# Kernel tuning notes

Measured on AMD Instinct MI355X. Metric: run time of the kernel, lower is better.

The kernel has to match this reference:

```python
import jax, jax.numpy as jnp
import numpy as np

DS = 32          # decoder_size
DIM = 512        # decoder_dim
NH = 8           # num_heads
HD = DIM // NH   # head_size = 64
NE = 4           # num_enc_reshape
NC = 2           # num_classes
B = 8
L = 2            # transformer layers
FF = 4 * DIM


def _ln(x, g, b):
    m = x.mean(-1, keepdims=True)
    v = x.var(-1, keepdims=True)
    return (x - m) / jnp.sqrt(v + 1e-5) * g + b


def _pos_bias(x_emb, y_emb, pad0, pad1):
    # 2D relative position encoding gathered from embeddings, shape [S2,S2,HD]
    ix = jnp.tile(jnp.arange(DS), DS)                       # column index per pixel
    iy = jnp.repeat(jnp.arange(DS), DS)                     # row index per pixel
    xd = jnp.clip(ix[None, :] - ix[:, None], -DS, DS) + DS  # [S2,S2] in [1,2*DS-1]
    yd = jnp.clip(iy[None, :] - iy[:, None], -DS, DS) + DS
    pos = x_emb[xd] + y_emb[yd]                              # [S2,S2,HD]
    S2 = DS * DS
    p0 = jnp.broadcast_to(pad0, (NE, NE, HD))
    p1 = jnp.broadcast_to(pad1, (S2, NE, HD))
    pos_pad = jnp.concatenate([p0, p1], axis=0)              # [S,NE,HD]
    right = jnp.concatenate([jnp.transpose(p1, (1, 0, 2)), pos], axis=0)  # [S,S2,HD]
    return jnp.concatenate([pos_pad, right], axis=1)         # [S,S,HD]


def _forward(x, patches, We, be, x_emb, y_emb, pad0, pad1,
             Wq, bq, Wk, bk, Wv, bv, Wo, bo,
             ln1_g, ln1_b, ln2_g, ln2_b, W1, b1, W2, b2, Wc, bc):
    b = x.shape[0]
    # patch embedding: [B,3,H,W] -> [B,H,W,3] -> Linear(3,DIM) -> [B,S2,DIM]
    p = jnp.transpose(patches, (0, 2, 3, 1))
    px = (p @ We + be).reshape(b, -1, DIM)
    xe = x.reshape(b, NE, DIM)
    h = jnp.concatenate([xe, px], axis=1)                    # [B,S,DIM]
    pos = _pos_bias(x_emb, y_emb, pad0, pad1)                # [S,S,HD]
    scale = 1.0 / jnp.sqrt(jnp.float32(HD))
    for l in range(L):
        hn = _ln(h, ln1_g[l], ln1_b[l])
        q = (hn @ Wq[l] + bq[l]).reshape(b, -1, NH, HD) * scale
        k = (hn @ Wk[l] + bk[l]).reshape(b, -1, NH, HD)
        v = (hn @ Wv[l] + bv[l]).reshape(b, -1, NH, HD)
        # content scores + gathered relative-position structure bias
        scores = jnp.einsum('bihd,bjhd->bhij', q, k) + jnp.einsum('bihd,ijd->bhij', q, pos)
        attn = jax.nn.softmax(scores, axis=-1)
        o = jnp.einsum('bhij,bjhd->bihd', attn, v).reshape(b, -1, DIM)
        h = h + (o @ Wo[l] + bo[l])
        hn = _ln(h, ln2_g[l], ln2_b[l])
        h = h + (jax.nn.relu(hn @ W1[l] + b1[l]) @ W2[l] + b2[l])
    out = h[:, NE:, :] @ Wc + bc                             # [B,S2,NC]
    out = out.reshape(b, DS, DS, NC)
    return jnp.transpose(out, (0, 3, 1, 2))                  # [B,NC,DS,DS]


def setup_inputs() -> dict:
    key = jax.random.key(0)
    ks = jax.random.split(key, 24)
    s = 0.02
    d = {}
    d['x'] = jax.random.normal(ks[0], (B, NE * DIM), jnp.float32)
    d['patches'] = jax.random.normal(ks[1], (B, 3, DS, DS), jnp.float32)
    d['We'] = jax.random.normal(ks[2], (3, DIM), jnp.float32) * s
    d['be'] = jnp.zeros((DIM,), jnp.float32)
    d['x_emb'] = jax.random.normal(ks[3], (2 * DS, HD), jnp.float32) * s
    d['y_emb'] = jax.random.normal(ks[4], (2 * DS, HD), jnp.float32) * s
    d['pad0'] = jax.random.normal(ks[5], (1, 1, HD), jnp.float32) * s
    d['pad1'] = jax.random.normal(ks[6], (1, 1, HD), jnp.float32) * s
    d['Wq'] = jax.random.normal(ks[7], (L, DIM, DIM), jnp.float32) * s
    d['bq'] = jnp.zeros((L, DIM), jnp.float32)
    d['Wk'] = jax.random.normal(ks[8], (L, DIM, DIM), jnp.float32) * s
    d['bk'] = jnp.zeros((L, DIM), jnp.float32)
    d['Wv'] = jax.random.normal(ks[9], (L, DIM, DIM), jnp.float32) * s
    d['bv'] = jnp.zeros((L, DIM), jnp.float32)
    d['Wo'] = jax.random.normal(ks[10], (L, DIM, DIM), jnp.float32) * s
    d['bo'] = jnp.zeros((L, DIM), jnp.float32)
    d['ln1_g'] = jnp.ones((L, DIM), jnp.float32)
    d['ln1_b'] = jnp.zeros((L, DIM), jnp.float32)
    d['ln2_g'] = jnp.ones((L, DIM), jnp.float32)
    d['ln2_b'] = jnp.zeros((L, DIM), jnp.float32)
    d['W1'] = jax.random.normal(ks[11], (L, DIM, FF), jnp.float32) * s
    d['b1'] = jnp.zeros((L, FF), jnp.float32)
    d['W2'] = jax.random.normal(ks[12], (L, FF, DIM), jnp.float32) * s
    d['b2'] = jnp.zeros((L, DIM), jnp.float32)
    d['Wc'] = jax.random.normal(ks[13], (DIM, NC), jnp.float32) * s
    d['bc'] = jnp.zeros((NC,), jnp.float32)
    return d


def reference(x, patches, We, be, x_emb, y_emb, pad0, pad1,
              Wq, bq, Wk, bk, Wv, bv, Wo, bo,
              ln1_g, ln1_b, ln2_g, ln2_b, W1, b1, W2, b2, Wc, bc):
    return _forward(x, patches, We, be, x_emb, y_emb, pad0, pad1,
                    Wq, bq, Wk, bk, Wv, bv, Wo, bo,
                    ln1_g, ln1_b, ln2_g, ln2_b, W1, b1, W2, b2, Wc, bc)
```

## Files before the change

kernel.cpp:

```cpp
#include <hip/hip_runtime.h>
#include <hip/hip_bf16.h>

#define DS 32
#define DIM 512
#define NH 8
#define HD 64
#define NE 4
#define NC 2
#define BB 8
#define LL 2
#define FFD 2048
#define S2 1024
#define SS 1028
#define MM (BB*SS)
#define KE 160
#define EXT ((size_t)BB*NH*SS*KE)

typedef __attribute__((ext_vector_type(8))) short s16x8;
typedef __attribute__((ext_vector_type(4))) float f32x4;
typedef unsigned short u16;

__device__ __forceinline__ u16 f2b(float f) {
    __hip_bfloat16 h = __float2bfloat16(f);
    return *reinterpret_cast<u16*>(&h);
}
__device__ __forceinline__ float b2f(u16 u) {
    __hip_bfloat16 h;
    *reinterpret_cast<u16*>(&h) = u;
    return __bfloat162float(h);
}

__device__ __forceinline__ void gload_lds16(const void* g, void* l) {
    __builtin_amdgcn_global_load_lds(
        (const __attribute__((address_space(1))) void*)(uintptr_t)g,
        (__attribute__((address_space(3))) void*)(uint32_t)(uintptr_t)l,
        16, 0, 0);
}

__global__ void embed_kernel(const float* __restrict__ x, const float* __restrict__ patches,
                             const float* __restrict__ We, const float* __restrict__ be,
                             float* __restrict__ h) {
    int row = blockIdx.x;
    int b = row / SS, i = row % SS;
    float* hr = h + (size_t)row * DIM;
    if (i < NE) {
        const float* xr = x + (size_t)b*NE*DIM + (size_t)i*DIM;
        for (int d = threadIdx.x; d < DIM; d += blockDim.x) hr[d] = xr[d];
    } else {
        int p = i - NE;
        float c0 = patches[(size_t)b*3*S2 + 0*S2 + p];
        float c1 = patches[(size_t)b*3*S2 + 1*S2 + p];
        float c2 = patches[(size_t)b*3*S2 + 2*S2 + p];
        for (int d = threadIdx.x; d < DIM; d += blockDim.x)
            hr[d] = be[d] + c0*We[d] + c1*We[DIM+d] + c2*We[2*DIM+d];
    }
}

__global__ void ln_kernel(const float* __restrict__ in, u16* __restrict__ out,
                          const float* __restrict__ g, const float* __restrict__ bt) {
    int row = blockIdx.x;
    const float* xr = in + (size_t)row*DIM;
    int t = threadIdx.x;
    float v0 = xr[t], v1 = xr[t+256];
    float s = v0 + v1, s2 = v0*v0 + v1*v1;
    for (int off = 32; off; off >>= 1) { s += __shfl_down(s, off); s2 += __shfl_down(s2, off); }
    __shared__ float ps[4], ps2[4];
    int wid = t >> 6, lane = t & 63;
    if (lane == 0) { ps[wid] = s; ps2[wid] = s2; }
    __syncthreads();
    if (t == 0) { ps[0] = ps[0]+ps[1]+ps[2]+ps[3]; ps2[0] = ps2[0]+ps2[1]+ps2[2]+ps2[3]; }
    __syncthreads();
    float mean = ps[0] * (1.0f/DIM);
    float var  = ps2[0] * (1.0f/DIM) - mean*mean;
    float inv = rsqrtf(var + 1e-5f);
    u16* orow = out + (size_t)row*DIM;
    orow[t]     = f2b((v0 - mean)*inv*g[t]     + bt[t]);
    orow[t+256] = f2b((v1 - mean)*inv*g[t+256] + bt[t+256]);
}

__global__ void transp_kernel(const float* __restrict__ src, u16* __restrict__ dst,
                              int R, int C) {
    __shared__ float tile[32][33];
    int c0 = blockIdx.x*32, r0 = blockIdx.y*32;
    int tx = threadIdx.x & 31, ty = threadIdx.x >> 5;
    #pragma unroll
    for (int ii = 0; ii < 4; ii++)
        tile[ty + ii*8][tx] = src[(size_t)(r0 + ty + ii*8)*C + c0 + tx];
    __syncthreads();
    #pragma unroll
    for (int ii = 0; ii < 4; ii++)
        dst[(size_t)(c0 + ty + ii*8)*R + r0 + tx] = f2b(tile[tx][ty + ii*8]);
}

__global__ void cat_bias_kernel(const float* __restrict__ bq, const float* __restrict__ bk,
                                const float* __restrict__ bv, float* __restrict__ out) {
    int t = blockIdx.x*256 + threadIdx.x;
    if (t >= 1536) return;
    out[t] = (t < 512) ? bq[t] : (t < 1024 ? bk[t-512] : bv[t-1024]);
}

template<int MODE, int RELU>
__global__ __launch_bounds__(256) void mfma_gemm(
    const u16* __restrict__ A, const u16* __restrict__ WT,
    const float* __restrict__ bias, const float* __restrict__ res,
    float* __restrict__ Cf, u16* __restrict__ Cb,
    u16* __restrict__ kd, u16* __restrict__ vd,
    int M, int N, int K, int Nt)
{
    __shared__ __align__(16) u16 a_lds[128*64];
    __shared__ __align__(16) u16 b_lds[128*64];
    int nwg = gridDim.x;
    int q8 = nwg >> 3, r8 = nwg & 7;
    int bid = blockIdx.x;
    int xcd = bid & 7, loc = bid >> 3;
    int g = (xcd < r8 ? xcd*(q8+1) : r8*(q8+1) + (xcd - r8)*q8) + loc;
    int row0 = (g / Nt) * 128, col0 = (g % Nt) * 128;

    int tid = threadIdx.x, w = tid>>6, l = tid&63;
    int lg = l>>4, lc = l&15;
    int wr = (w>>1)*64, wc = (w&1)*64;
    f32x4 acc[4][4];
    #pragma unroll
    for (int m = 0; m < 4; m++)
        #pragma unroll
        for (int n = 0; n < 4; n++) { f32x4 z = {0.f,0.f,0.f,0.f}; acc[m][n] = z; }

    int c16 = l & 7;
    for (int k0 = 0; k0 < K; k0 += 64) {
        #pragma unroll
        for (int p = 0; p < 4; p++) {
            int e = p*256 + tid;
            int r = e >> 3;
            int ra = row0 + r; if (ra > M-1) ra = M-1;
            gload_lds16(A  + (size_t)ra*K + k0 + c16*8,          a_lds + p*2048 + w*512);
            gload_lds16(WT + (size_t)(col0 + r)*K + k0 + c16*8,  b_lds + p*2048 + w*512);
        }
        __syncthreads();
        #pragma unroll
        for (int ks = 0; ks < 2; ks++) {
            int cb = ks*32 + lg*8;
            s16x8 af[4], bfr[4];
            #pragma unroll
            for (int m = 0; m < 4; m++)
                af[m] = *(const s16x8*)(a_lds + (wr + m*16 + lc)*64 + cb);
            #pragma unroll
            for (int n = 0; n < 4; n++)
                bfr[n] = *(const s16x8*)(b_lds + (wc + n*16 + lc)*64 + cb);
            #pragma unroll
            for (int m = 0; m < 4; m++)
                #pragma unroll
                for (int n = 0; n < 4; n++)
                    acc[m][n] = __builtin_amdgcn_mfma_f32_16x16x32_bf16(af[m], bfr[n], acc[m][n], 0, 0, 0);
        }
        __syncthreads();
    }
    #pragma unroll
    for (int m = 0; m < 4; m++) {
        #pragma unroll
        for (int r = 0; r < 4; r++) {
            int row = row0 + wr + m*16 + lg*4 + r;
            if (row >= M) continue;
            #pragma unroll
            for (int n = 0; n < 4; n++) {
                int col = col0 + wc + n*16 + lc;
                float v = acc[m][n][r] + bias[col];
                if (MODE == 2) {
                    int which = col >> 9, c2 = col & 511;
                    if (which == 0) v *= 0.125f;
                    u16* dst = (which == 0) ? Cb : (which == 1 ? kd : vd);
                    dst[(size_t)row*512 + c2] = f2b(v);
                } else if (MODE == 1) {
                    if (RELU) v = fmaxf(v, 0.f);
                    Cb[(size_t)row*N + col] = f2b(v);
                } else {
                    Cf[(size_t)row*N + col] = v + res[(size_t)row*N + col];
                }
            }
        }
    }
}

__global__ void qp_kernel(const u16* __restrict__ q, const float* __restrict__ pad0,
                          const float* __restrict__ pad1, float* __restrict__ qp0,
                          float* __restrict__ qp1) {
    int idx = blockIdx.x * blockDim.x + threadIdx.x;
    if (idx >= BB*NH*SS) return;
    int i = idx % SS; int bh = idx / SS; int b = bh >> 3, hh = bh & 7;
    const u16* qr = q + ((size_t)(b*SS + i))*DIM + hh*HD;
    float a0 = 0.f, a1 = 0.f;
    #pragma unroll 8
    for (int d = 0; d < HD; d++) { float qv = b2f(qr[d]); a0 += qv*pad0[d]; a1 += qv*pad1[d]; }
    qp0[idx] = a0; qp1[idx] = a1;
}

__global__ void qext_kernel(const u16* __restrict__ qb, const float* __restrict__ qp0,
                            const float* __restrict__ qp1, u16* __restrict__ Qe) {
    size_t id = (size_t)blockIdx.x*256 + threadIdx.x;
    if (id >= EXT/8) return;
    int u = (int)(id % 20);
    size_t row = id / 20;
    int bh = (int)(row / SS), i = (int)(row - (size_t)bh*SS);
    int b = bh >> 3, hh = bh & 7;
    s16x8 val = {0,0,0,0,0,0,0,0};
    if (u < 8) {
        val = *(const s16x8*)(qb + ((size_t)(b*SS + i))*DIM + hh*HD + u*8);
    } else if (u == 16) {
        float v128 = (i < NE) ? qp0[bh*SS + i] : qp1[bh*SS + i];
        float v129 = (i < NE) ? qp1[bh*SS + i] : 0.f;
        val[0] = (short)f2b(v128);
        val[1] = (short)f2b(v129);
    }
    *(s16x8*)(Qe + row*KE + u*8) = val;
}

__global__ void kext_kernel(const u16* __restrict__ kb, u16* __restrict__ Ke) {
    size_t id = (size_t)blockIdx.x*256 + threadIdx.x;
    if (id >= EXT/8) return;
    int u = (int)(id % 20);
    size_t row = id / 20;
    int bh = (int)(row / SS), j = (int)(row - (size_t)bh*SS);
    int b = bh >> 3, hh = bh & 7;
    const short ONE = 0x3F80;
    s16x8 val = {0,0,0,0,0,0,0,0};
    if (u < 8) {
        val = *(const s16x8*)(kb + ((size_t)(b*SS + j))*DIM + hh*HD + u*8);
    } else {
        int pj = j - NE, cj = pj & 31, rj = pj >> 5;
        #pragma unroll
        for (int e = 0; e < 8; e++) {
            int t = u*8 + e;
            short v = 0;
            if (j >= NE) {
                if (t < 96)       { if (cj == t-64) v = ONE; }
                else if (t < 128) { if (rj == t-96) v = ONE; }
                else if (t == 129) v = ONE;
            } else if (t == 128) v = ONE;
            val[e] = v;
        }
    }
    *(s16x8*)(Ke + row*KE + u*8) = val;
}

__global__ __launch_bounds__(256) void qxy_mfma(
    const u16* __restrict__ q, const float* __restrict__ x_emb,
    const float* __restrict__ y_emb, u16* __restrict__ Qe)
{
    int tile = blockIdx.x, bh = blockIdx.y;
    int b = bh >> 3, hh = bh & 7;
    int tid = threadIdx.x, w = tid>>6, l = tid&63;
    int lg = l>>4, lc = l&15;
    int wr = (w>>1)*64, wc = (w&1)*64;
    int pi0 = tile*128;

    f32x4 acc[4][4];
    #pragma unroll
    for (int m = 0; m < 4; m++)
        #pragma unroll
        for (int n = 0; n < 4; n++) { f32x4 z = {0.f,0.f,0.f,0.f}; acc[m][n] = z; }

    s16x8 af[4][2];
    #pragma unroll
    for (int m = 0; m < 4; m++) {
        int pi = pi0 + wr + m*16 + lc;
        const u16* qp = q + ((size_t)(b*SS + NE + pi))*DIM + hh*HD + lg*8;
        af[m][0] = *(const s16x8*)qp;
        af[m][1] = *(const s16x8*)(qp + 32);
    }
    s16x8 bf[4][2];
    #pragma unroll
    for (int n = 0; n < 4; n++) {
        int tau = wc + n*16 + lc;
        const float* ep = (tau < 64) ? (x_emb + (size_t)tau*HD) : (y_emb + (size_t)(tau-64)*HD);
        #pragma unroll
        for (int ks = 0; ks < 2; ks++) {
            const float* e8 = ep + ks*32 + lg*8;
            s16x8 bv;
            #pragma unroll
            for (int t2 = 0; t2 < 8; t2++) bv[t2] = (short)f2b(e8[t2]);
            bf[n][ks] = bv;
        }
    }
    #pragma unroll
    for (int ks = 0; ks < 2; ks++)
        #pragma unroll
        for (int m = 0; m < 4; m++)
            #pragma unroll
            for (int n = 0; n < 4; n++)
                acc[m][n] = __builtin_amdgcn_mfma_f32_16x16x32_bf16(af[m][ks], bf[n][ks], acc[m][n], 0, 0, 0);

    #pragma unroll
    for (int m = 0; m < 4; m++) {
        #pragma unroll
        for (int r = 0; r < 4; r++) {
            int pi = pi0 + wr + m*16 + lg*4 + r;
            int ci = pi & 31, ri = pi >> 5;
            size_t rowbase = ((size_t)bh*SS + NE + pi)*KE;
            #pragma unroll
            for (int n = 0; n < 4; n++) {
                int tau = wc + n*16 + lc;
                float v = acc[m][n][r];
                if (tau < 64) {
                    int c = tau + ci - 32;
                    if (c >= 0 && c < 32) Qe[rowbase + 64 + c] = f2b(v);
                } else {
                    int c = (tau - 64) + ri - 32;
                    if (c >= 0 && c < 32) Qe[rowbase + 96 + c] = f2b(v);
                }
            }
        }
    }
}

#define KT2 128
#define NKT2 9
#define NQT 17
__global__ __launch_bounds__(256) void attn_mfma(
    const u16* __restrict__ Qe, const u16* __restrict__ Ke,
    const u16* __restrict__ v, u16* __restrict__ o)
{
    __shared__ __align__(16) u16 Kl[128*192];
    __shared__ __align__(16) u16 Vt[2][64][72];
    __shared__ __align__(16) u16 Pl[4][16][72];
    int bid = blockIdx.x;
    int g = (bid & 7)*136 + (bid >> 3);
    int qt = g % NQT, bh = g / NQT;
    int b = bh >> 3, hh = bh & 7;
    int tid = threadIdx.x, w = tid>>6, l = tid&63;
    int lg = l>>4, lc = l&15;
    int i0w = qt*64 + w*16;
    const s16x8 zs = {0,0,0,0,0,0,0,0};

    s16x8 qa[5];
    {
        int qrow = i0w + lc; if (qrow > SS-1) qrow = SS-1;
        const u16* qp = Qe + ((size_t)bh*SS + qrow)*KE + lg*8;
        #pragma unroll
        for (int ks = 0; ks < 5; ks++) qa[ks] = *(const s16x8*)(qp + ks*32);
    }

    float m_[4] = {-1e30f, -1e30f, -1e30f, -1e30f};
    float l_[4] = {0.f, 0.f, 0.f, 0.f};
    f32x4 oacc[4];
    #pragma unroll
    for (int f = 0; f < 4; f++) { f32x4 z = {0.f,0.f,0.f,0.f}; oacc[f] = z; }

    int skey = tid & 63, sd0 = (tid >> 6) * 16;

    for (int kt2 = 0; kt2 < NKT2; kt2++) {
        int j0 = kt2 * KT2;
        #pragma unroll
        for (int p = 0; p < 10; p++) {
            int e = p*256 + tid;
            int row = e / 20, u = e - row*20;
            int j = j0 + row;
            s16x8 kv = zs;
            if (j < SS) kv = *(const s16x8*)(Ke + ((size_t)bh*SS + j)*KE + u*8);
            *(s16x8*)((char*)Kl + row*384 + ((u ^ (row&7)) << 4)) = kv;
        }
        #pragma unroll
        for (int hb = 0; hb < 2; hb++) {
            int key = j0 + hb*64 + skey;
            uint4 v0 = {0,0,0,0}, v1 = {0,0,0,0};
            if (key < SS) {
                const uint4* vp = (const uint4*)(v + ((size_t)(b*SS + key))*DIM + hh*HD + sd0);
                v0 = vp[0]; v1 = vp[1];
            }
            const u16* pv = (const u16*)&v0;
            #pragma unroll
            for (int jj = 0; jj < 8; jj++) Vt[hb][sd0 + jj][skey] = pv[jj];
            pv = (const u16*)&v1;
            #pragma unroll
            for (int jj = 0; jj < 8; jj++) Vt[hb][sd0 + 8 + jj][skey] = pv[jj];
        }
        __syncthreads();

        f32x4 s[8];
        #pragma unroll
        for (int f = 0; f < 8; f++) { f32x4 z = {0.f,0.f,0.f,0.f}; s[f] = z; }
        #pragma unroll
        for (int ks = 0; ks < 5; ks++)
            #pragma unroll
            for (int f = 0; f < 8; f++) {
                int row = f*16 + lc;
                s16x8 kb2 = *(const s16x8*)((const char*)Kl + row*384 + ((((ks<<2)+lg) ^ (row&7)) << 4));
                s[f] = __builtin_amdgcn_mfma_f32_16x16x32_bf16(qa[ks], kb2, s[f], 0, 0, 0);
            }

        #pragma unroll
        for (int r = 0; r < 4; r++) {
            #pragma unroll
            for (int f = 0; f < 8; f++) {
                int j = j0 + f*16 + lc;
                if (j >= SS) s[f][r] = -1e30f;
            }
            float t4 = fmaxf(fmaxf(fmaxf(s[0][r], s[1][r]), fmaxf(s[2][r], s[3][r])),
                             fmaxf(fmaxf(s[4][r], s[5][r]), fmaxf(s[6][r], s[7][r])));
            t4 = fmaxf(t4, __shfl_xor(t4, 1));
            t4 = fmaxf(t4, __shfl_xor(t4, 2));
            t4 = fmaxf(t4, __shfl_xor(t4, 4));
            t4 = fmaxf(t4, __shfl_xor(t4, 8));
            float mn = fmaxf(m_[r], t4);
            float sc = __expf(m_[r] - mn);
            m_[r] = mn;
            float rs = 0.f;
            #pragma unroll
            for (int f = 0; f < 8; f++) {
                float p = __expf(s[f][r] - mn);
                s[f][r] = p;
                rs += p;
            }
            rs += __shfl_xor(rs, 1); rs += __shfl_xor(rs, 2);
            rs += __shfl_xor(rs, 4); rs += __shfl_xor(rs, 8);
            l_[r] = l_[r]*sc + rs;
            #pragma unroll
            for (int f = 0; f < 4; f++) oacc[f][r] *= sc;
        }
        #pragma unroll
        for (int hb = 0; hb < 2; hb++) {
            #pragma unroll
            for (int r = 0; r < 4; r++)
                #pragma unroll
                for (int f = 0; f < 4; f++)
                    Pl[w][lg*4 + r][f*16 + lc] = f2b(s[hb*4 + f][r]);
            #pragma unroll
            for (int ks = 0; ks < 2; ks++) {
                s16x8 pa = *(const s16x8*)&Pl[w][lc][ks*32 + lg*8];
                #pragma unroll
                for (int f = 0; f < 4; f++) {
                    s16x8 vb = *(const s16x8*)&Vt[hb][f*16 + lc][ks*32 + lg*8];
                    oacc[f] = __builtin_amdgcn_mfma_f32_16x16x32_bf16(pa, vb, oacc[f], 0, 0, 0);
                }
            }
        }
        __syncthreads();
    }
    #pragma unroll
    for (int r = 0; r < 4; r++) {
        int i = i0w + lg*4 + r;
        if (i >= SS) continue;
        float inv = 1.0f / l_[r];
        #pragma unroll
        for (int f = 0; f < 4; f++)
            o[((size_t)(b*SS + i))*DIM + hh*HD + f*16 + lc] = f2b(oacc[f][r] * inv);
    }
}

__global__ void cls_kernel(const float* __restrict__ h, const float* __restrict__ Wc,
                           const float* __restrict__ bc, float* __restrict__ out) {
    int g = blockIdx.x*4 + (threadIdx.x >> 6);
    int lane = threadIdx.x & 63;
    if (g >= BB*S2) return;
    int b = g >> 10, p = g & 1023;
    const float* hr = h + ((size_t)(b*SS + NE + p))*DIM;
    float a0 = 0.f, a1 = 0.f;
    for (int d = lane; d < DIM; d += 64) {
        float hv = hr[d];
        a0 += hv * Wc[d*NC + 0];
        a1 += hv * Wc[d*NC + 1];
    }
    for (int off = 32; off; off >>= 1) { a0 += __shfl_down(a0, off); a1 += __shfl_down(a1, off); }
    if (lane == 0) {
        out[((size_t)(b*NC + 0))*S2 + p] = a0 + bc[0];
        out[((size_t)(b*NC + 1))*S2 + p] = a1 + bc[1];
    }
}

extern "C" void kernel_launch(void* const* d_in, const int* in_sizes, int n_in,
                              void* d_out, int out_size, void* d_ws, size_t ws_size,
                              hipStream_t stream) {
    const float* x      = (const float*)d_in[0];
    const float* patches= (const float*)d_in[1];
    const float* We     = (const float*)d_in[2];
    const float* be     = (const float*)d_in[3];
    const float* x_emb  = (const float*)d_in[4];
    const float* y_emb  = (const float*)d_in[5];
    const float* pad0   = (const float*)d_in[6];
    const float* pad1   = (const float*)d_in[7];
    const float* Wq     = (const float*)d_in[8];
    const float* bq     = (const float*)d_in[9];
    const float* Wk     = (const float*)d_in[10];
    const float* bk     = (const float*)d_in[11];
    const float* Wv     = (const float*)d_in[12];
    const float* bv     = (const float*)d_in[13];
    const float* Wo     = (const float*)d_in[14];
    const float* bo     = (const float*)d_in[15];
    const float* ln1_g  = (const float*)d_in[16];
    const float* ln1_b  = (const float*)d_in[17];
    const float* ln2_g  = (const float*)d_in[18];
    const float* ln2_b  = (const float*)d_in[19];
    const float* W1     = (const float*)d_in[20];
    const float* b1     = (const float*)d_in[21];
    const float* W2     = (const float*)d_in[22];
    const float* b2     = (const float*)d_in[23];
    const float* Wc     = (const float*)d_in[24];
    const float* bc     = (const float*)d_in[25];
    float* out = (float*)d_out;

    float* ws = (float*)d_ws;
    const size_t MD = (size_t)MM*DIM;
    float* h  = ws;
    u16* hn   = (u16*)(ws + MD);
    u16* qb   = (u16*)(ws + MD + MD/2);
    u16* kb   = qb + MD;
    u16* vb   = qb + 2*MD;
    u16* ob   = qb + 3*MD;
    u16* tb   = qb;
    u16* Qe   = (u16*)(ws + 3*MD + MD/2);
    u16* Ke   = Qe + EXT;
    float* after = ws + 3*MD + MD/2 + EXT;
    float* qp0 = after;
    float* qp1 = qp0 + 65792;
    float* bqkv = qp1 + 65792;
    u16* wt   = (u16*)(bqkv + 1536);

    const size_t WL = 3145728;

    for (int l = 0; l < LL; l++) {
        u16* base = wt + (size_t)l*WL;
        transp_kernel<<<dim3(16,16), 256, 0, stream>>>(Wq + (size_t)l*DIM*DIM, base + 0,        DIM, DIM);
        transp_kernel<<<dim3(16,16), 256, 0, stream>>>(Wk + (size_t)l*DIM*DIM, base + 262144,   DIM, DIM);
        transp_kernel<<<dim3(16,16), 256, 0, stream>>>(Wv + (size_t)l*DIM*DIM, base + 524288,   DIM, DIM);
        transp_kernel<<<dim3(16,16), 256, 0, stream>>>(Wo + (size_t)l*DIM*DIM, base + 786432,   DIM, DIM);
        transp_kernel<<<dim3(64,16), 256, 0, stream>>>(W1 + (size_t)l*DIM*FFD, base + 1048576,  DIM, FFD);
        transp_kernel<<<dim3(16,64), 256, 0, stream>>>(W2 + (size_t)l*FFD*DIM, base + 2097152,  FFD, DIM);
    }

    embed_kernel<<<MM, 256, 0, stream>>>(x, patches, We, be, h);

    const int extUnits = (int)(EXT / 8);
    const int extBlocks = (extUnits + 255) / 256;

    for (int l = 0; l < LL; l++) {
        u16* base = wt + (size_t)l*WL;
        cat_bias_kernel<<<6, 256, 0, stream>>>(bq + (size_t)l*DIM, bk + (size_t)l*DIM, bv + (size_t)l*DIM, bqkv);
        ln_kernel<<<MM, 256, 0, stream>>>(h, hn, ln1_g + l*DIM, ln1_b + l*DIM);
        mfma_gemm<2,0><<<65*12, 256, 0, stream>>>(hn, base, bqkv, nullptr, nullptr, qb, kb, vb, MM, 1536, DIM, 12);
        qp_kernel<<<(BB*NH*SS + 255)/256, 256, 0, stream>>>(qb, pad0, pad1, qp0, qp1);
        qext_kernel<<<extBlocks, 256, 0, stream>>>(qb, qp0, qp1, Qe);
        qxy_mfma<<<dim3(8, BB*NH), 256, 0, stream>>>(qb, x_emb, y_emb, Qe);
        kext_kernel<<<extBlocks, 256, 0, stream>>>(kb, Ke);
        attn_mfma<<<NQT*BB*NH, 256, 0, stream>>>(Qe, Ke, vb, ob);
        mfma_gemm<0,0><<<65*4, 256, 0, stream>>>(ob, base + 786432, bo + (size_t)l*DIM, h, h, nullptr, nullptr, nullptr, MM, DIM, DIM, 4);
        ln_kernel<<<MM, 256, 0, stream>>>(h, hn, ln2_g + l*DIM, ln2_b + l*DIM);
        mfma_gemm<1,1><<<65*16, 256, 0, stream>>>(hn, base + 1048576, b1 + (size_t)l*FFD, nullptr, nullptr, tb, nullptr, nullptr, MM, FFD, DIM, 16);
        mfma_gemm<0,0><<<65*4, 256, 0, stream>>>(tb, base + 2097152, b2 + (size_t)l*DIM, h, h, nullptr, nullptr, nullptr, MM, DIM, FFD, 4);
    }

    cls_kernel<<<(BB*S2)/4, 256, 0, stream>>>(h, Wc, bc, out);
}
```

Measured before the change: 860.2 us.

## Double-buffer GEMM LDS tiles and shrink attention key tile to 64

The MFMA GEMM now uses two LDS buffers per operand and issues global-to-LDS loads for the next K tile before computing the current one, so load latency overlaps with MFMA work. Separately, the attention kernel processes 64 keys per iteration instead of 128, which shrinks its LDS footprint and score registers. The cost is 64KB of LDS in the GEMM, which may limit occupancy, and twice as many barriers and softmax rescales in attention.

```diff
diff --git a/kernel.cpp b/kernel.cpp
--- a/kernel.cpp
+++ b/kernel.cpp
@@ -107,8 +107,8 @@
     u16* __restrict__ kd, u16* __restrict__ vd,
     int M, int N, int K, int Nt)
 {
-    __shared__ __align__(16) u16 a_lds[128*64];
-    __shared__ __align__(16) u16 b_lds[128*64];
+    __shared__ __align__(16) u16 a_lds[2][128*64];
+    __shared__ __align__(16) u16 b_lds[2][128*64];
     int nwg = gridDim.x;
     int q8 = nwg >> 3, r8 = nwg & 7;
     int bid = blockIdx.x;
@@ -126,26 +126,33 @@
         for (int n = 0; n < 4; n++) { f32x4 z = {0.f,0.f,0.f,0.f}; acc[m][n] = z; }
 
     int c16 = l & 7;
-    for (int k0 = 0; k0 < K; k0 += 64) {
+    auto STAGE = [&](int buf, int kk) {
         #pragma unroll
         for (int p = 0; p < 4; p++) {
             int e = p*256 + tid;
             int r = e >> 3;
             int ra = row0 + r; if (ra > M-1) ra = M-1;
-            gload_lds16(A  + (size_t)ra*K + k0 + c16*8,          a_lds + p*2048 + w*512);
-            gload_lds16(WT + (size_t)(col0 + r)*K + k0 + c16*8,  b_lds + p*2048 + w*512);
-        }
-        __syncthreads();
+            gload_lds16(A  + (size_t)ra*K + kk + c16*8,          a_lds[buf] + p*2048 + w*512);
+            gload_lds16(WT + (size_t)(col0 + r)*K + kk + c16*8,  b_lds[buf] + p*2048 + w*512);
+        }
+    };
+
+    STAGE(0, 0);
+    __syncthreads();
+    int nk = K >> 6;
+    for (int ki = 0; ki < nk; ki++) {
+        int cur = ki & 1;
+        if (ki + 1 < nk) STAGE(cur ^ 1, (ki + 1) << 6);
         #pragma unroll
         for (int ks = 0; ks < 2; ks++) {
             int cb = ks*32 + lg*8;
             s16x8 af[4], bfr[4];
             #pragma unroll
             for (int m = 0; m < 4; m++)
-                af[m] = *(const s16x8*)(a_lds + (wr + m*16 + lc)*64 + cb);
+                af[m] = *(const s16x8*)(a_lds[cur] + (wr + m*16 + lc)*64 + cb);
             #pragma unroll
             for (int n = 0; n < 4; n++)
-                bfr[n] = *(const s16x8*)(b_lds + (wc + n*16 + lc)*64 + cb);
+                bfr[n] = *(const s16x8*)(b_lds[cur] + (wc + n*16 + lc)*64 + cb);
             #pragma unroll
             for (int m = 0; m < 4; m++)
                 #pragma unroll
@@ -311,15 +318,15 @@
     }
 }
 
-#define KT2 128
-#define NKT2 9
+#define KT 64
+#define NKT 17
 #define NQT 17
 __global__ __launch_bounds__(256) void attn_mfma(
     const u16* __restrict__ Qe, const u16* __restrict__ Ke,
     const u16* __restrict__ v, u16* __restrict__ o)
 {
-    __shared__ __align__(16) u16 Kl[128*192];
-    __shared__ __align__(16) u16 Vt[2][64][72];
+    __shared__ __align__(16) u16 Kl[64*192];
+    __shared__ __align__(16) u16 Vt[64][72];
     __shared__ __align__(16) u16 Pl[4][16][72];
     int bid = blockIdx.x;
     int g = (bid & 7)*136 + (bid >> 3);
@@ -346,10 +353,10 @@
 
     int skey = tid & 63, sd0 = (tid >> 6) * 16;
 
-    for (int kt2 = 0; kt2 < NKT2; kt2++) {
-        int j0 = kt2 * KT2;
-        #pragma unroll
-        for (int p = 0; p < 10; p++) {
+    for (int kt2 = 0; kt2 < NKT; kt2++) {
+        int j0 = kt2 * KT;
+        #pragma unroll
+        for (int p = 0; p < 5; p++) {
             int e = p*256 + tid;
             int row = e / 20, u = e - row*20;
             int j = j0 + row;
@@ -357,9 +364,8 @@
             if (j < SS) kv = *(const s16x8*)(Ke + ((size_t)bh*SS + j)*KE + u*8);
             *(s16x8*)((char*)Kl + row*384 + ((u ^ (row&7)) << 4)) = kv;
         }
-        #pragma unroll
-        for (int hb = 0; hb < 2; hb++) {
-            int key = j0 + hb*64 + skey;
+        {
+            int key = j0 + skey;
             uint4 v0 = {0,0,0,0}, v1 = {0,0,0,0};
             if (key < SS) {
                 const uint4* vp = (const uint4*)(v + ((size_t)(b*SS + key))*DIM + hh*HD + sd0);
@@ -367,20 +373,20 @@
             }
             const u16* pv = (const u16*)&v0;
             #pragma unroll
-            for (int jj = 0; jj < 8; jj++) Vt[hb][sd0 + jj][skey] = pv[jj];
+            for (int jj = 0; jj < 8; jj++) Vt[sd0 + jj][skey] = pv[jj];
             pv = (const u16*)&v1;
             #pragma unroll
-            for (int jj = 0; jj < 8; jj++) Vt[hb][sd0 + 8 + jj][skey] = pv[jj];
+            for (int jj = 0; jj < 8; jj++) Vt[sd0 + 8 + jj][skey] = pv[jj];
         }
         __syncthreads();
 
-        f32x4 s[8];
-        #pragma unroll
-        for (int f = 0; f < 8; f++) { f32x4 z = {0.f,0.f,0.f,0.f}; s[f] = z; }
+        f32x4 s[4];
+        #pragma unroll
+        for (int f = 0; f < 4; f++) { f32x4 z = {0.f,0.f,0.f,0.f}; s[f] = z; }
         #pragma unroll
         for (int ks = 0; ks < 5; ks++)
             #pragma unroll
-            for (int f = 0; f < 8; f++) {
+            for (int f = 0; f < 4; f++) {
                 int row = f*16 + lc;
                 s16x8 kb2 = *(const s16x8*)((const char*)Kl + row*384 + ((((ks<<2)+lg) ^ (row&7)) << 4));
                 s[f] = __builtin_amdgcn_mfma_f32_16x16x32_bf16(qa[ks], kb2, s[f], 0, 0, 0);
@@ -389,12 +395,11 @@
         #pragma unroll
         for (int r = 0; r < 4; r++) {
             #pragma unroll
-            for (int f = 0; f < 8; f++) {
+            for (int f = 0; f < 4; f++) {
                 int j = j0 + f*16 + lc;
                 if (j >= SS) s[f][r] = -1e30f;
             }
-            float t4 = fmaxf(fmaxf(fmaxf(s[0][r], s[1][r]), fmaxf(s[2][r], s[3][r])),
-                             fmaxf(fmaxf(s[4][r], s[5][r]), fmaxf(s[6][r], s[7][r])));
+            float t4 = fmaxf(fmaxf(s[0][r], s[1][r]), fmaxf(s[2][r], s[3][r]));
             t4 = fmaxf(t4, __shfl_xor(t4, 1));
             t4 = fmaxf(t4, __shfl_xor(t4, 2));
             t4 = fmaxf(t4, __shfl_xor(t4, 4));
@@ -404,7 +409,7 @@
             m_[r] = mn;
             float rs = 0.f;
             #pragma unroll
-            for (int f = 0; f < 8; f++) {
+            for (int f = 0; f < 4; f++) {
                 float p = __expf(s[f][r] - mn);
                 s[f][r] = p;
                 rs += p;
@@ -416,20 +421,17 @@
             for (int f = 0; f < 4; f++) oacc[f][r] *= sc;
         }
         #pragma unroll
-        for (int hb = 0; hb < 2; hb++) {
-            #pragma unroll
-            for (int r = 0; r < 4; r++)
-                #pragma unroll
-                for (int f = 0; f < 4; f++)
-                    Pl[w][lg*4 + r][f*16 + lc] = f2b(s[hb*4 + f][r]);
-            #pragma unroll
-            for (int ks = 0; ks < 2; ks++) {
-                s16x8 pa = *(const s16x8*)&Pl[w][lc][ks*32 + lg*8];
-                #pragma unroll
-                for (int f = 0; f < 4; f++) {
-                    s16x8 vb = *(const s16x8*)&Vt[hb][f*16 + lc][ks*32 + lg*8];
-                    oacc[f] = __builtin_amdgcn_mfma_f32_16x16x32_bf16(pa, vb, oacc[f], 0, 0, 0);
-                }
+        for (int r = 0; r < 4; r++)
+            #pragma unroll
+            for (int f = 0; f < 4; f++)
+                Pl[w][lg*4 + r][f*16 + lc] = f2b(s[f][r]);
+        #pragma unroll
+        for (int ks = 0; ks < 2; ks++) {
+            s16x8 pa = *(const s16x8*)&Pl[w][lc][ks*32 + lg*8];
+            #pragma unroll
+            for (int f = 0; f < 4; f++) {
+                s16x8 vb = *(const s16x8*)&Vt[f*16 + lc][ks*32 + lg*8];
+                oacc[f] = __builtin_amdgcn_mfma_f32_16x16x32_bf16(pa, vb, oacc[f], 0, 0, 0);
             }
         }
         __syncthreads();
```

Result: faster. 727.5 us (-15.4%).
